# Kernel tuning notes

Measured on AMD Instinct MI355X. Metric: run time of the kernel, lower is better.

The kernel has to match this reference:

```python
import jax, jax.numpy as jnp
import numpy as np

B, N, D, P, H = 16, 1024, 512, 512, 8
E = P // H  # head dim = 64


def layer_norm(x, g, b, eps=1e-5):
    mu = jnp.mean(x, axis=-1, keepdims=True)
    var = jnp.var(x, axis=-1, keepdims=True)
    return (x - mu) * jax.lax.rsqrt(var + eps) * g + b


def setup_inputs() -> dict:
    key = jax.random.key(0)
    ks = jax.random.split(key, 12)
    s = 0.02
    inp = {
        "x": jax.random.normal(ks[0], (B, N, D), dtype=jnp.float32),
        "Wq": jax.random.normal(ks[1], (D, P), dtype=jnp.float32) * s,
        "bq": jnp.zeros((P,), jnp.float32),
        "Wk": jax.random.normal(ks[2], (D, P), dtype=jnp.float32) * s,
        "bk": jnp.zeros((P,), jnp.float32),
        "Wv": jax.random.normal(ks[3], (D, P), dtype=jnp.float32) * s,
        "bv": jnp.zeros((P,), jnp.float32),
        "Wo": jax.random.normal(ks[4], (P, D), dtype=jnp.float32) * s,
        "bo": jnp.zeros((D,), jnp.float32),
        "ln1_g": jnp.ones((D,), jnp.float32),
        "ln1_b": jnp.zeros((D,), jnp.float32),
        "W1": jax.random.normal(ks[5], (D, 4 * D), dtype=jnp.float32) * s,
        "b1": jnp.zeros((4 * D,), jnp.float32),
        "W2": jax.random.normal(ks[6], (4 * D, D), dtype=jnp.float32) * s,
        "b2": jnp.zeros((D,), jnp.float32),
        "ln2_g": jnp.ones((D,), jnp.float32),
        "ln2_b": jnp.zeros((D,), jnp.float32),
    }
    return inp


def reference(x, Wq, bq, Wk, bk, Wv, bv, Wo, bo, ln1_g, ln1_b, W1, b1, W2, b2, ln2_g, ln2_b):
    # dropout layers are identity in eval mode
    q = (x @ Wq + bq).reshape(B, N, H, E)
    k = (x @ Wk + bk).reshape(B, N, H, E)
    v = (x @ Wv + bv).reshape(B, N, H, E)
    scale = 1.0 / jnp.sqrt(jnp.float32(E))
    scores = jnp.einsum('blhe,bshe->bhls', q, k)  # [B,H,L,S]
    A = jax.nn.softmax(scale * scores, axis=-1)
    V = jnp.einsum('bhls,bshd->blhd', A, v).reshape(B, N, P)
    att = V @ Wo + bo
    x1 = layer_norm(x + att, ln1_g, ln1_b)
    # FFN: 1x1 convs over channel dim == per-token linears, exact GELU
    ff = jax.nn.gelu(x1 @ W1 + b1, approximate=False) @ W2 + b2
    return layer_norm(x1 + ff, ln2_g, ln2_b)
```

## Files before the change

kernel.cpp:

```cpp
#include <hip/hip_runtime.h>
#include <hip/hip_bf16.h>

typedef __hip_bfloat16 bf16;
typedef __bf16 bf16x8 __attribute__((ext_vector_type(8)));
typedef __bf16 bf16x4 __attribute__((ext_vector_type(4)));
typedef float f32x4 __attribute__((ext_vector_type(4)));

static __device__ __forceinline__ f32x4 mfma16(bf16x8 a, bf16x8 b, f32x4 c) {
  return __builtin_amdgcn_mfma_f32_16x16x32_bf16(a, b, c, 0, 0, 0);
}
static __device__ __forceinline__ bf16x8 ld8(const bf16* p) {
  return *reinterpret_cast<const bf16x8*>(p);
}

typedef __attribute__((address_space(1))) void gvoid;
typedef __attribute__((address_space(3))) void lvoid;
static __device__ __forceinline__ void gl2lds16(const bf16* g, bf16* l) {
  __builtin_amdgcn_global_load_lds((gvoid*)g, (lvoid*)l, 16, 0, 0);
}

__global__ __launch_bounds__(256) void cvt_prep(
    const float* __restrict__ x, bf16* __restrict__ xb,
    const float* __restrict__ Wq, const float* __restrict__ Wk,
    const float* __restrict__ Wv, const float* __restrict__ Wo,
    const float* __restrict__ W1, const float* __restrict__ W2,
    bf16* __restrict__ Wtqkv, bf16* __restrict__ WtO,
    bf16* __restrict__ Wt1, bf16* __restrict__ Wt2) {
  int blk = blockIdx.x;
  int tx = threadIdx.x, ty = threadIdx.y;
  if (blk < 8192) {
    int t = ty * 32 + tx;
    long i = (long)blk * 256 + t;
    float4 v = reinterpret_cast<const float4*>(x)[i];
    bf16x4 o;
    o[0] = __float2bfloat16(v.x); o[1] = __float2bfloat16(v.y);
    o[2] = __float2bfloat16(v.z); o[3] = __float2bfloat16(v.w);
    reinterpret_cast<bf16x4*>(xb)[i] = o;
    return;
  }
  int id = blk - 8192;
  const float* in;
  bf16* out;
  int K, N, n0, k0;
  if (id < 1024) {
    int which = id >> 8, t = id & 255;
    K = 512; N = 512;
    n0 = (t & 15) * 32; k0 = (t >> 4) * 32;
    if (which == 0)      { in = Wq; out = Wtqkv; }
    else if (which == 1) { in = Wk; out = Wtqkv + (size_t)512 * 512; }
    else if (which == 2) { in = Wv; out = Wtqkv + (size_t)1024 * 512; }
    else                 { in = Wo; out = WtO; }
  } else if (id < 2048) {
    int t = id - 1024;
    in = W1; out = Wt1; K = 512; N = 2048;
    n0 = (t & 63) * 32; k0 = (t >> 6) * 32;
  } else {
    int t = id - 2048;
    in = W2; out = Wt2; K = 2048; N = 512;
    n0 = (t & 15) * 32; k0 = (t >> 4) * 32;
  }
  __shared__ float tile[32][33];
#pragma unroll
  for (int j = 0; j < 32; j += 8)
    tile[ty + j][tx] = in[(long)(k0 + ty + j) * N + n0 + tx];
  __syncthreads();
#pragma unroll
  for (int j = 0; j < 32; j += 8)
    out[(long)(n0 + ty + j) * K + k0 + tx] = __float2bfloat16(tile[tx][ty + j]);
}

__global__ __launch_bounds__(256) void cvt_kernel(const float* __restrict__ in,
                                                  bf16* __restrict__ out) {
  long i = (long)blockIdx.x * 256 + threadIdx.x;
  float4 v = reinterpret_cast<const float4*>(in)[i];
  bf16x4 o;
  o[0] = __float2bfloat16(v.x); o[1] = __float2bfloat16(v.y);
  o[2] = __float2bfloat16(v.z); o[3] = __float2bfloat16(v.w);
  reinterpret_cast<bf16x4*>(out)[i] = o;
}

__global__ void prep_weights(const float* __restrict__ Wq, const float* __restrict__ Wk,
                             const float* __restrict__ Wv, const float* __restrict__ Wo,
                             const float* __restrict__ W1, const float* __restrict__ W2,
                             bf16* __restrict__ Wtqkv, bf16* __restrict__ WtO,
                             bf16* __restrict__ Wt1, bf16* __restrict__ Wt2) {
  int id = blockIdx.x;
  const float* in;
  bf16* out;
  int K, N, n0, k0;
  if (id < 1024) {
    int which = id >> 8, t = id & 255;
    K = 512; N = 512;
    n0 = (t & 15) * 32; k0 = (t >> 4) * 32;
    if (which == 0)      { in = Wq; out = Wtqkv; }
    else if (which == 1) { in = Wk; out = Wtqkv + (size_t)512 * 512; }
    else if (which == 2) { in = Wv; out = Wtqkv + (size_t)1024 * 512; }
    else                 { in = Wo; out = WtO; }
  } else if (id < 2048) {
    int t = id - 1024;
    in = W1; out = Wt1; K = 512; N = 2048;
    n0 = (t & 63) * 32; k0 = (t >> 6) * 32;
  } else {
    int t = id - 2048;
    in = W2; out = Wt2; K = 2048; N = 512;
    n0 = (t & 15) * 32; k0 = (t >> 4) * 32;
  }
  __shared__ float tile[32][33];
  int tx = threadIdx.x, ty = threadIdx.y;
#pragma unroll
  for (int j = 0; j < 32; j += 8)
    tile[ty + j][tx] = in[(long)(k0 + ty + j) * N + n0 + tx];
  __syncthreads();
#pragma unroll
  for (int j = 0; j < 32; j += 8)
    out[(long)(n0 + ty + j) * K + k0 + tx] = __float2bfloat16(tile[tx][ty + j]);
}

template <int MODE>
__global__ __launch_bounds__(256) void gemm_kernel(
    const bf16* __restrict__ A, const bf16* __restrict__ Wt,
    const float* __restrict__ b0, const float* __restrict__ b1_,
    const float* __restrict__ b2_, bf16* C0, bf16* C1, bf16* C2,
    int K, int ldc, int mmask, int mshift) {
  __shared__ alignas(16) bf16 As[3][128 * 32];
  __shared__ alignas(16) bf16 Bs[3][128 * 32];
  const int tid = threadIdx.x;
  const int wave = tid >> 6, lane = tid & 63;
  const int lr = lane & 15, lq = lane >> 4;
  const int L = blockIdx.x;
  const int m0 = (L & mmask) * 128, n0 = (L >> mshift) * 128;
  const int wm = (wave >> 1) * 64, wn = (wave & 1) * 64;

  const int srow0 = (wave * 2) * 16 + (lane >> 2);
  const int srow1 = (wave * 2 + 1) * 16 + (lane >> 2);
  const int scol = (lane & 3) * 8;
  const bf16* Ag0 = A + (long)(m0 + srow0) * K + scol;
  const bf16* Ag1 = A + (long)(m0 + srow1) * K + scol;
  const bf16* Bg0 = Wt + (long)(n0 + srow0) * K + scol;
  const bf16* Bg1 = Wt + (long)(n0 + srow1) * K + scol;
  const int so0 = (wave * 2) * 16 * 32;
  const int so1 = (wave * 2 + 1) * 16 * 32;

  f32x4 acc[4][4] = {};

  auto stage = [&](int k0, int buf) {
    gl2lds16(Ag0 + k0, &As[buf][so0]);
    gl2lds16(Ag1 + k0, &As[buf][so1]);
    gl2lds16(Bg0 + k0, &Bs[buf][so0]);
    gl2lds16(Bg1 + k0, &Bs[buf][so1]);
  };

  stage(0, 0);
  stage(32, 1);

  const int nk = K >> 5;
  int cur = 0, sb = 2;
  for (int t = 0; t < nk; ++t) {
    if (t < nk - 1) {
      asm volatile("s_waitcnt vmcnt(4)" ::: "memory");
    } else {
      asm volatile("s_waitcnt vmcnt(0)" ::: "memory");
    }
    __builtin_amdgcn_s_barrier();
    if (t < nk - 2) stage((t + 2) << 5, sb);

    bf16x8 af[4], bfr[4];
#pragma unroll
    for (int i = 0; i < 4; ++i) af[i] = ld8(&As[cur][(wm + i * 16 + lr) * 32 + lq * 8]);
#pragma unroll
    for (int j = 0; j < 4; ++j) bfr[j] = ld8(&Bs[cur][(wn + j * 16 + lr) * 32 + lq * 8]);
    if constexpr (MODE == 3) {
#pragma unroll
      for (int i = 0; i < 4; ++i)
#pragma unroll
        for (int j = 0; j < 4; ++j) acc[i][j] = mfma16(af[i], bfr[j], acc[i][j]);
    } else {
#pragma unroll
      for (int i = 0; i < 4; ++i)
#pragma unroll
        for (int j = 0; j < 4; ++j) acc[i][j] = mfma16(bfr[j], af[i], acc[i][j]);
    }

    cur = (cur == 2) ? 0 : cur + 1;
    sb = (sb == 2) ? 0 : sb + 1;
  }

  if constexpr (MODE == 3) {
#pragma unroll
    for (int i = 0; i < 4; ++i) {
      int row0 = m0 + wm + i * 16 + lq * 4;
      int bb = row0 >> 10, tok = row0 & 1023;
#pragma unroll
      for (int j = 0; j < 4; ++j) {
        int col = n0 + wn + j * 16 + lr;
        float bv = b0[col];
        int hh = col >> 6, e = col & 63;
        bf16x4 o;
#pragma unroll
        for (int rr = 0; rr < 4; ++rr) o[rr] = __float2bfloat16(acc[i][j][rr] + bv);
        *reinterpret_cast<bf16x4*>(
            &C0[(((long)((bb * 8 + hh) * 64 + e)) << 10) + tok]) = o;
      }
    }
  } else {
    const float* bias = b0;
    bf16* C = C0;
    int cb = n0;
    if (MODE == 2 && n0 >= 512) { bias = b1_; C = C1; cb = n0 - 512; }
#pragma unroll
    for (int i = 0; i < 4; ++i) {
      int row = m0 + wm + i * 16 + lr;
      long rb = (long)row * ldc;
#pragma unroll
      for (int j = 0; j < 4; ++j) {
        int col0 = cb + wn + j * 16 + lq * 4;
        f32x4 bv = *reinterpret_cast<const f32x4*>(&bias[col0]);
        bf16x4 o;
#pragma unroll
        for (int rr = 0; rr < 4; ++rr) {
          float v = acc[i][j][rr] + bv[rr];
          if (MODE == 1) v = 0.5f * v * (1.0f + erff(v * 0.70710678118654752f));
          o[rr] = __float2bfloat16(v);
        }
        *reinterpret_cast<bf16x4*>(&C[rb + col0]) = o;
      }
    }
  }
}

__global__ __launch_bounds__(256) void attn_fused(
    const bf16* __restrict__ Q, const bf16* __restrict__ Km,
    const bf16* __restrict__ Vt, bf16* __restrict__ O) {
  constexpr int SP = 72;
  __shared__ alignas(16) bf16 Pall[4][32 * SP];
  __shared__ alignas(16) bf16 Ks[2][2][64][32];
  __shared__ alignas(16) bf16 Vs[2][2][64][32];
  const int tid = threadIdx.x;
  const int wave = tid >> 6, lane = tid & 63;
  const int lr = lane & 15, lq = lane >> 4;
  const int L = blockIdx.x;
  const int bh = ((L >> 6) << 3) | (L & 7);
  const int qc = (L >> 3) & 7;
  const int h = bh & 7, b = bh >> 3;
  const int q0 = qc * 128 + wave * 32;
  bf16* P = Pall[wave];
  const float Cc = 0.18033688011112042f;

  bf16x8 qf[2][2];
#pragma unroll
  for (int qs = 0; qs < 2; ++qs) {
    const bf16* qrow = Q + (long)(b * 1024 + q0 + qs * 16 + lr) * 512 + h * 64;
    qf[qs][0] = ld8(qrow + lq * 8);
    qf[qs][1] = ld8(qrow + 32 + lq * 8);
  }
  const bf16* kbase = Km + (long)(b * 1024) * 512 + h * 64;
  const bf16* vbase = Vt + (long)((b * 8 + h) * 64) * 1024;

  const int sr = wave * 16 + (lane >> 2);
  const int sc = (lane & 3) * 8;
  const bf16* Kg = kbase + (long)sr * 512 + sc;
  const bf16* Vg = vbase + (long)sr * 1024 + sc;

  auto stage = [&](int kb, int p) {
#pragma unroll
    for (int kk = 0; kk < 2; ++kk)
      gl2lds16(Kg + (long)kb * 64 * 512 + kk * 32, &Ks[p][kk][wave * 16][0]);
#pragma unroll
    for (int kk = 0; kk < 2; ++kk)
      gl2lds16(Vg + kb * 64 + kk * 32, &Vs[p][kk][wave * 16][0]);
  };

  bf16x8 ones;
#pragma unroll
  for (int k = 0; k < 8; ++k) ones[k] = __float2bfloat16(1.0f);

  f32x4 oacc[2][4] = {};
  f32x4 lacc[2] = {};

  stage(0, 0);
  __syncthreads();

  int p = 0;
  for (int kb = 0; kb < 16; ++kb) {
    if (kb < 15) stage(kb + 1, p ^ 1);
#pragma unroll
    for (int kt = 0; kt < 4; ++kt) {
      bf16x8 kf0 = ld8(&Ks[p][0][kt * 16 + lr][lq * 8]);
      bf16x8 kf1 = ld8(&Ks[p][1][kt * 16 + lr][lq * 8]);
#pragma unroll
      for (int qs = 0; qs < 2; ++qs) {
        f32x4 t = {};
        t = mfma16(kf0, qf[qs][0], t);
        t = mfma16(kf1, qf[qs][1], t);
        bf16x4 pk;
#pragma unroll
        for (int rr = 0; rr < 4; ++rr) pk[rr] = __float2bfloat16(exp2f(t[rr] * Cc));
        *reinterpret_cast<bf16x4*>(&P[(qs * 16 + lr) * SP + kt * 16 + lq * 4]) = pk;
      }
    }
    __builtin_amdgcn_sched_barrier(0);
    bf16x8 pf[2][2];
#pragma unroll
    for (int qs = 0; qs < 2; ++qs) {
      pf[qs][0] = ld8(&P[(qs * 16 + lr) * SP + lq * 8]);
      pf[qs][1] = ld8(&P[(qs * 16 + lr) * SP + 32 + lq * 8]);
    }
#pragma unroll
    for (int qs = 0; qs < 2; ++qs) {
      lacc[qs] = mfma16(ones, pf[qs][0], lacc[qs]);
      lacc[qs] = mfma16(ones, pf[qs][1], lacc[qs]);
    }
#pragma unroll
    for (int j0 = 0; j0 < 4; ++j0) {
      bf16x8 vf0 = ld8(&Vs[p][0][j0 * 16 + lr][lq * 8]);
      bf16x8 vf1 = ld8(&Vs[p][1][j0 * 16 + lr][lq * 8]);
#pragma unroll
      for (int qs = 0; qs < 2; ++qs) {
        oacc[qs][j0] = mfma16(vf0, pf[qs][0], oacc[qs][j0]);
        oacc[qs][j0] = mfma16(vf1, pf[qs][1], oacc[qs][j0]);
      }
    }
    __builtin_amdgcn_sched_barrier(0);
    __syncthreads();
    p ^= 1;
  }

#pragma unroll
  for (int qs = 0; qs < 2; ++qs) {
    float lv = 1.0f / lacc[qs][0];
    bf16* orow = O + (long)(b * 1024 + q0 + qs * 16 + lr) * 512 + h * 64 + lq * 4;
#pragma unroll
    for (int j0 = 0; j0 < 4; ++j0) {
      bf16x4 o;
#pragma unroll
      for (int rr = 0; rr < 4; ++rr) o[rr] = __float2bfloat16(oacc[qs][j0][rr] * lv);
      *reinterpret_cast<bf16x4*>(&orow[j0 * 16]) = o;
    }
  }
}

__global__ __launch_bounds__(256) void attn_kernel(
    const bf16* Q, const bf16* __restrict__ Km,
    const bf16* __restrict__ Vt, bf16* O) {
  constexpr int SP = 72;
  __shared__ alignas(16) bf16 Pall[4][64 * SP];
  const int tid = threadIdx.x;
  const int wave = tid >> 6, lane = tid & 63;
  const int lr = lane & 15, lq = lane >> 4;
  const int L = blockIdx.x;
  const int bh = ((L >> 5) << 3) | (L & 7);
  const int qc = (L >> 3) & 3;
  const int h = bh & 7, b = bh >> 3;
  const int q0 = qc * 256 + wave * 64;
  bf16* P = Pall[wave];
  const float Cc = 0.18033688011112042f;

  bf16x8 qf[4][2];
#pragma unroll
  for (int qs = 0; qs < 4; ++qs) {
    const bf16* qrow = Q + (long)(b * 1024 + q0 + qs * 16 + lr) * 512 + h * 64;
    qf[qs][0] = ld8(qrow + lq * 8);
    qf[qs][1] = ld8(qrow + 32 + lq * 8);
  }
  const bf16* kbase = Km + (long)(b * 1024) * 512 + h * 64;
  const bf16* vbase = Vt + (long)((b * 8 + h) * 64) * 1024;

  bf16x8 ones;
#pragma unroll
  for (int k = 0; k < 8; ++k) ones[k] = __float2bfloat16(1.0f);

  f32x4 oacc[4][4] = {};
  f32x4 lacc[4] = {};

  for (int kb = 0; kb < 16; ++kb) {
#pragma unroll
    for (int kt = 0; kt < 4; ++kt) {
      const bf16* krow = kbase + (long)(kb * 64 + kt * 16 + lr) * 512;
      bf16x8 kf0 = ld8(krow + lq * 8);
      bf16x8 kf1 = ld8(krow + 32 + lq * 8);
#pragma unroll
      for (int qs = 0; qs < 4; ++qs) {
        f32x4 t = {};
        t = mfma16(kf0, qf[qs][0], t);
        t = mfma16(kf1, qf[qs][1], t);
        bf16x4 pk;
#pragma unroll
        for (int rr = 0; rr < 4; ++rr) pk[rr] = __float2bfloat16(exp2f(t[rr] * Cc));
        *reinterpret_cast<bf16x4*>(&P[(qs * 16 + lr) * SP + kt * 16 + lq * 4]) = pk;
      }
    }
    __builtin_amdgcn_sched_barrier(0);
    bf16x8 pf[4][2];
#pragma unroll
    for (int qs = 0; qs < 4; ++qs) {
      pf[qs][0] = ld8(&P[(qs * 16 + lr) * SP + lq * 8]);
      pf[qs][1] = ld8(&P[(qs * 16 + lr) * SP + 32 + lq * 8]);
    }
#pragma unroll
    for (int qs = 0; qs < 4; ++qs) {
      lacc[qs] = mfma16(pf[qs][0], ones, lacc[qs]);
      lacc[qs] = mfma16(pf[qs][1], ones, lacc[qs]);
    }
#pragma unroll
    for (int j0 = 0; j0 < 4; ++j0) {
      const bf16* vrow = vbase + (long)(j0 * 16 + lr) * 1024 + kb * 64;
      bf16x8 vf0 = ld8(vrow + lq * 8);
      bf16x8 vf1 = ld8(vrow + 32 + lq * 8);
#pragma unroll
      for (int qs = 0; qs < 4; ++qs) {
        oacc[qs][j0] = mfma16(pf[qs][0], vf0, oacc[qs][j0]);
        oacc[qs][j0] = mfma16(pf[qs][1], vf1, oacc[qs][j0]);
      }
    }
    __builtin_amdgcn_sched_barrier(0);
  }

#pragma unroll
  for (int qs = 0; qs < 4; ++qs)
#pragma unroll
    for (int rr = 0; rr < 4; ++rr) {
      float lv = 1.0f / lacc[qs][rr];
#pragma unroll
      for (int j0 = 0; j0 < 4; ++j0)
        O[(long)(b * 1024 + q0 + qs * 16 + lq * 4 + rr) * 512 + h * 64 + j0 * 16 + lr] =
            __float2bfloat16(oacc[qs][j0][rr] * lv);
    }
}

template <typename TO>
__global__ __launch_bounds__(256) void add_ln_kernel(
    const bf16* __restrict__ X, const bf16* __restrict__ Y,
    const float* __restrict__ g, const float* __restrict__ bb,
    TO* __restrict__ out) {
  const int lane = threadIdx.x & 63, wave = threadIdx.x >> 6;
  const long row = (long)blockIdx.x * 4 + wave;
  const long base = row * 512 + lane * 8;
  bf16x8 xv = ld8(X + base);
  bf16x8 yv = ld8(Y + base);
  float v[8];
  float s = 0.f, q = 0.f;
#pragma unroll
  for (int k = 0; k < 8; ++k) {
    v[k] = (float)xv[k] + (float)yv[k];
    s += v[k];
    q += v[k] * v[k];
  }
#pragma unroll
  for (int o = 32; o > 0; o >>= 1) {
    s += __shfl_down(s, o);
    q += __shfl_down(q, o);
  }
  s = __shfl(s, 0);
  q = __shfl(q, 0);
  float mean = s * (1.f / 512.f);
  float var = q * (1.f / 512.f) - mean * mean;
  float rs = rsqrtf(var + 1e-5f);
  f32x4 g0 = *reinterpret_cast<const f32x4*>(&g[lane * 8]);
  f32x4 g1 = *reinterpret_cast<const f32x4*>(&g[lane * 8 + 4]);
  f32x4 b0 = *reinterpret_cast<const f32x4*>(&bb[lane * 8]);
  f32x4 b1 = *reinterpret_cast<const f32x4*>(&bb[lane * 8 + 4]);
  float r[8];
#pragma unroll
  for (int k = 0; k < 4; ++k) {
    r[k]     = (v[k]     - mean) * rs * g0[k] + b0[k];
    r[k + 4] = (v[k + 4] - mean) * rs * g1[k] + b1[k];
  }
  if constexpr (sizeof(TO) == 2) {
    bf16x8 o;
#pragma unroll
    for (int k = 0; k < 8; ++k) o[k] = __float2bfloat16(r[k]);
    *reinterpret_cast<bf16x8*>(&out[base]) = o;
  } else {
    f32x4 o0, o1;
#pragma unroll
    for (int k = 0; k < 4; ++k) { o0[k] = r[k]; o1[k] = r[k + 4]; }
    *reinterpret_cast<f32x4*>(&out[base]) = o0;
    *reinterpret_cast<f32x4*>(&out[base + 4]) = o1;
  }
}

extern "C" void kernel_launch(void* const* d_in, const int* in_sizes, int n_in,
                              void* d_out, int out_size, void* d_ws, size_t ws_size,
                              hipStream_t stream) {
  const float* x    = (const float*)d_in[0];
  const float* Wq   = (const float*)d_in[1];
  const float* bq   = (const float*)d_in[2];
  const float* Wk   = (const float*)d_in[3];
  const float* bk   = (const float*)d_in[4];
  const float* Wv   = (const float*)d_in[5];
  const float* bv   = (const float*)d_in[6];
  const float* Wo   = (const float*)d_in[7];
  const float* bo   = (const float*)d_in[8];
  const float* ln1g = (const float*)d_in[9];
  const float* ln1b = (const float*)d_in[10];
  const float* W1   = (const float*)d_in[11];
  const float* b1   = (const float*)d_in[12];
  const float* W2   = (const float*)d_in[13];
  const float* b2   = (const float*)d_in[14];
  const float* ln2g = (const float*)d_in[15];
  const float* ln2b = (const float*)d_in[16];
  float* out = (float*)d_out;

  char* ws = (char*)d_ws;
  size_t off = 0;
  auto alloc = [&](size_t bytes) {
    char* p = ws + off;
    off += (bytes + 255) & ~(size_t)255;
    return (bf16*)p;
  };
  bf16* Wtqkv = alloc((size_t)1536 * 512 * 2);
  bf16* WtO   = alloc((size_t)512 * 512 * 2);
  bf16* Wt1   = alloc((size_t)512 * 2048 * 2);
  bf16* Wt2   = alloc((size_t)2048 * 512 * 2);
  const size_t SB = (size_t)16384 * 512 * 2;

  dim3 tb(32, 8);

  if (ws_size >= (size_t)104 * 1024 * 1024) {
    bf16* xb  = alloc(SB);
    bf16* kb  = alloc(SB);
    bf16* qb  = alloc(SB);
    bf16* vtb = alloc(SB);
    bf16* p0  = alloc(SB);
    bf16* p1  = alloc(SB);
    bf16* ff1 = qb;
    bf16* ff2 = xb;
    (void)p0; (void)p1;

    cvt_prep<<<11264, tb, 0, stream>>>(x, xb, Wq, Wk, Wv, Wo, W1, W2,
                                       Wtqkv, WtO, Wt1, Wt2);
    gemm_kernel<2><<<1024, 256, 0, stream>>>(xb, Wtqkv, bq, bk, nullptr,
                                             qb, kb, nullptr, 512, 512, 127, 7);
    gemm_kernel<3><<<512, 256, 0, stream>>>(xb, Wtqkv + (size_t)1024 * 512, bv,
                                            nullptr, nullptr, vtb, nullptr, nullptr,
                                            512, 512, 127, 7);
    attn_fused<<<1024, 256, 0, stream>>>(qb, kb, vtb, qb);
    gemm_kernel<0><<<512, 256, 0, stream>>>(qb, WtO, bo, nullptr, nullptr,
                                            vtb, nullptr, nullptr, 512, 512, 127, 7);
    add_ln_kernel<bf16><<<4096, 256, 0, stream>>>(xb, vtb, ln1g, ln1b, kb);
    gemm_kernel<1><<<2048, 256, 0, stream>>>(kb, Wt1, b1, nullptr, nullptr,
                                             ff1, nullptr, nullptr, 512, 2048, 127, 7);
    gemm_kernel<0><<<512, 256, 0, stream>>>(ff1, Wt2, b2, nullptr, nullptr,
                                            ff2, nullptr, nullptr, 2048, 512, 127, 7);
    add_ln_kernel<float><<<4096, 256, 0, stream>>>(kb, ff2, ln2g, ln2b, out);
  } else {
    bf16* xb  = alloc(SB);
    bf16* kb  = alloc(SB);
    bf16* qb  = alloc(SB);
    bf16* vtb = alloc(SB);
    bf16* fb  = alloc(SB / 2);
    bf16* ff1 = qb;

    cvt_kernel<<<8192, 256, 0, stream>>>(x, xb);
    prep_weights<<<3072, tb, 0, stream>>>(Wq, Wk, Wv, Wo, W1, W2,
                                          Wtqkv, WtO, Wt1, Wt2);
    gemm_kernel<2><<<1024, 256, 0, stream>>>(xb, Wtqkv, bq, bk, nullptr,
                                             qb, kb, nullptr, 512, 512, 127, 7);
    gemm_kernel<3><<<512, 256, 0, stream>>>(xb, Wtqkv + (size_t)1024 * 512, bv,
                                            nullptr, nullptr, vtb, nullptr, nullptr,
                                            512, 512, 127, 7);
    attn_kernel<<<512, 256, 0, stream>>>(qb, kb, vtb, qb);
    gemm_kernel<0><<<512, 256, 0, stream>>>(qb, WtO, bo, nullptr, nullptr,
                                            vtb, nullptr, nullptr, 512, 512, 127, 7);
    add_ln_kernel<bf16><<<4096, 256, 0, stream>>>(xb, vtb, ln1g, ln1b, kb);

    for (int hh = 0; hh < 2; ++hh) {
      const bf16* x1h = kb + (size_t)hh * 8192 * 512;
      gemm_kernel<1><<<1024, 256, 0, stream>>>(x1h, Wt1, b1, nullptr, nullptr,
                                               ff1, nullptr, nullptr, 512, 2048, 63, 6);
      gemm_kernel<0><<<256, 256, 0, stream>>>(ff1, Wt2, b2, nullptr, nullptr,
                                              fb, nullptr, nullptr, 2048, 512, 63, 6);
      add_ln_kernel<float><<<2048, 256, 0, stream>>>(x1h, fb, ln2g, ln2b,
                                                     out + (size_t)hh * 8192 * 512);
    }
  }
}
```

Before: 368.9 us.

## Add 256x256 GEMM tile kernel and fold softmax scale into Wq

Adds a 512-thread GEMM kernel with 256x256 output tiles and a three-stage LDS pipeline, used for the QK projection and the FFN up-projection with GELU. Larger tiles raise reuse per LDS load and cut the number of blocks. The softmax scale (log2e/sqrt(E)) is now folded into Wq and bq during weight prep, which removes a multiply per score in the attention kernels. Risks are lower occupancy and more register pressure from the 8x4 accumulator tile, and fewer blocks (256) for the QK GEMM than there are CUs.

```diff
diff --git a/kernel.cpp b/kernel.cpp
--- a/kernel.cpp
+++ b/kernel.cpp
@@ -18,12 +18,15 @@
 static __device__ __forceinline__ void gl2lds16(const bf16* g, bf16* l) {
   __builtin_amdgcn_global_load_lds((gvoid*)g, (lvoid*)l, 16, 0, 0);
 }
+
+#define CC_SCALE 0.18033688011112042f
 
 __global__ __launch_bounds__(256) void cvt_prep(
     const float* __restrict__ x, bf16* __restrict__ xb,
     const float* __restrict__ Wq, const float* __restrict__ Wk,
     const float* __restrict__ Wv, const float* __restrict__ Wo,
     const float* __restrict__ W1, const float* __restrict__ W2,
+    const float* __restrict__ bq, float* __restrict__ bqs,
     bf16* __restrict__ Wtqkv, bf16* __restrict__ WtO,
     bf16* __restrict__ Wt1, bf16* __restrict__ Wt2) {
   int blk = blockIdx.x;
@@ -38,15 +41,22 @@
     reinterpret_cast<bf16x4*>(xb)[i] = o;
     return;
   }
+  if (blk == 11264) {
+    int t = ty * 32 + tx;
+    bqs[t] = bq[t] * CC_SCALE;
+    bqs[t + 256] = bq[t + 256] * CC_SCALE;
+    return;
+  }
   int id = blk - 8192;
   const float* in;
   bf16* out;
   int K, N, n0, k0;
+  float scl = 1.0f;
   if (id < 1024) {
     int which = id >> 8, t = id & 255;
     K = 512; N = 512;
     n0 = (t & 15) * 32; k0 = (t >> 4) * 32;
-    if (which == 0)      { in = Wq; out = Wtqkv; }
+    if (which == 0)      { in = Wq; out = Wtqkv; scl = CC_SCALE; }
     else if (which == 1) { in = Wk; out = Wtqkv + (size_t)512 * 512; }
     else if (which == 2) { in = Wv; out = Wtqkv + (size_t)1024 * 512; }
     else                 { in = Wo; out = WtO; }
@@ -66,7 +76,7 @@
   __syncthreads();
 #pragma unroll
   for (int j = 0; j < 32; j += 8)
-    out[(long)(n0 + ty + j) * K + k0 + tx] = __float2bfloat16(tile[tx][ty + j]);
+    out[(long)(n0 + ty + j) * K + k0 + tx] = __float2bfloat16(tile[tx][ty + j] * scl);
 }
 
 __global__ __launch_bounds__(256) void cvt_kernel(const float* __restrict__ in,
@@ -82,17 +92,25 @@
 __global__ void prep_weights(const float* __restrict__ Wq, const float* __restrict__ Wk,
                              const float* __restrict__ Wv, const float* __restrict__ Wo,
                              const float* __restrict__ W1, const float* __restrict__ W2,
+                             const float* __restrict__ bq, float* __restrict__ bqs,
                              bf16* __restrict__ Wtqkv, bf16* __restrict__ WtO,
                              bf16* __restrict__ Wt1, bf16* __restrict__ Wt2) {
   int id = blockIdx.x;
+  int tx = threadIdx.x, ty = threadIdx.y;
+  if (id == 0) {
+    int t = ty * 32 + tx;
+    bqs[t] = bq[t] * CC_SCALE;
+    bqs[t + 256] = bq[t + 256] * CC_SCALE;
+  }
   const float* in;
   bf16* out;
   int K, N, n0, k0;
+  float scl = 1.0f;
   if (id < 1024) {
     int which = id >> 8, t = id & 255;
     K = 512; N = 512;
     n0 = (t & 15) * 32; k0 = (t >> 4) * 32;
-    if (which == 0)      { in = Wq; out = Wtqkv; }
+    if (which == 0)      { in = Wq; out = Wtqkv; scl = CC_SCALE; }
     else if (which == 1) { in = Wk; out = Wtqkv + (size_t)512 * 512; }
     else if (which == 2) { in = Wv; out = Wtqkv + (size_t)1024 * 512; }
     else                 { in = Wo; out = WtO; }
@@ -106,14 +124,13 @@
     n0 = (t & 15) * 32; k0 = (t >> 4) * 32;
   }
   __shared__ float tile[32][33];
-  int tx = threadIdx.x, ty = threadIdx.y;
 #pragma unroll
   for (int j = 0; j < 32; j += 8)
     tile[ty + j][tx] = in[(long)(k0 + ty + j) * N + n0 + tx];
   __syncthreads();
 #pragma unroll
   for (int j = 0; j < 32; j += 8)
-    out[(long)(n0 + ty + j) * K + k0 + tx] = __float2bfloat16(tile[tx][ty + j]);
+    out[(long)(n0 + ty + j) * K + k0 + tx] = __float2bfloat16(tile[tx][ty + j] * scl);
 }
 
 template <int MODE>
@@ -224,6 +241,90 @@
         }
         *reinterpret_cast<bf16x4*>(&C[rb + col0]) = o;
       }
+    }
+  }
+}
+
+template <int MODE>
+__global__ __launch_bounds__(512) void gemm256(
+    const bf16* __restrict__ A, const bf16* __restrict__ Wt,
+    const float* __restrict__ b0, const float* __restrict__ b1_,
+    bf16* C0, bf16* C1, int K, int ldc, int mmask, int mshift) {
+  __shared__ alignas(16) bf16 As[3][256 * 32];
+  __shared__ alignas(16) bf16 Bs[3][256 * 32];
+  const int tid = threadIdx.x;
+  const int wave = tid >> 6, lane = tid & 63;
+  const int lr = lane & 15, lq = lane >> 4;
+  const int L = blockIdx.x;
+  const int m0 = (L & mmask) * 256, n0 = (L >> mshift) * 256;
+  const int wm = (wave >> 2) * 128, wn = (wave & 3) * 64;
+
+  const int sr = tid >> 2;
+  const int sc = (tid & 3) * 8;
+  const bf16* Ag0 = A + (long)(m0 + sr) * K + sc;
+  const bf16* Ag1 = A + (long)(m0 + 128 + sr) * K + sc;
+  const bf16* Bg0 = Wt + (long)(n0 + sr) * K + sc;
+  const bf16* Bg1 = Wt + (long)(n0 + 128 + sr) * K + sc;
+  const int so0 = tid * 8;
+  const int so1 = (tid + 512) * 8;
+
+  f32x4 acc[8][4] = {};
+
+  auto stage = [&](int k0, int buf) {
+    gl2lds16(Ag0 + k0, &As[buf][so0]);
+    gl2lds16(Ag1 + k0, &As[buf][so1]);
+    gl2lds16(Bg0 + k0, &Bs[buf][so0]);
+    gl2lds16(Bg1 + k0, &Bs[buf][so1]);
+  };
+
+  stage(0, 0);
+  stage(32, 1);
+
+  const int nk = K >> 5;
+  int cur = 0, sb = 2;
+  for (int t = 0; t < nk; ++t) {
+    if (t < nk - 1) {
+      asm volatile("s_waitcnt vmcnt(4)" ::: "memory");
+    } else {
+      asm volatile("s_waitcnt vmcnt(0)" ::: "memory");
+    }
+    __builtin_amdgcn_s_barrier();
+    if (t < nk - 2) stage((t + 2) << 5, sb);
+
+    bf16x8 af[8], bfr[4];
+#pragma unroll
+    for (int i = 0; i < 8; ++i) af[i] = ld8(&As[cur][(wm + i * 16 + lr) * 32 + lq * 8]);
+#pragma unroll
+    for (int j = 0; j < 4; ++j) bfr[j] = ld8(&Bs[cur][(wn + j * 16 + lr) * 32 + lq * 8]);
+#pragma unroll
+    for (int i = 0; i < 8; ++i)
+#pragma unroll
+      for (int j = 0; j < 4; ++j) acc[i][j] = mfma16(bfr[j], af[i], acc[i][j]);
+
+    cur = (cur == 2) ? 0 : cur + 1;
+    sb = (sb == 2) ? 0 : sb + 1;
+  }
+
+  const float* bias = b0;
+  bf16* C = C0;
+  int cb = n0;
+  if (MODE == 2 && n0 >= 512) { bias = b1_; C = C1; cb = n0 - 512; }
+#pragma unroll
+  for (int i = 0; i < 8; ++i) {
+    int row = m0 + wm + i * 16 + lr;
+    long rb = (long)row * ldc;
+#pragma unroll
+    for (int j = 0; j < 4; ++j) {
+      int col0 = cb + wn + j * 16 + lq * 4;
+      f32x4 bv = *reinterpret_cast<const f32x4*>(&bias[col0]);
+      bf16x4 o;
+#pragma unroll
+      for (int rr = 0; rr < 4; ++rr) {
+        float v = acc[i][j][rr] + bv[rr];
+        if (MODE == 1) v = 0.5f * v * (1.0f + erff(v * 0.70710678118654752f));
+        o[rr] = __float2bfloat16(v);
+      }
+      *reinterpret_cast<bf16x4*>(&C[rb + col0]) = o;
     }
   }
 }
@@ -244,7 +345,6 @@
   const int h = bh & 7, b = bh >> 3;
   const int q0 = qc * 128 + wave * 32;
   bf16* P = Pall[wave];
-  const float Cc = 0.18033688011112042f;
 
   bf16x8 qf[2][2];
 #pragma unroll
@@ -294,7 +394,7 @@
         t = mfma16(kf1, qf[qs][1], t);
         bf16x4 pk;
 #pragma unroll
-        for (int rr = 0; rr < 4; ++rr) pk[rr] = __float2bfloat16(exp2f(t[rr] * Cc));
+        for (int rr = 0; rr < 4; ++rr) pk[rr] = __float2bfloat16(exp2f(t[rr]));
         *reinterpret_cast<bf16x4*>(&P[(qs * 16 + lr) * SP + kt * 16 + lq * 4]) = pk;
       }
     }
@@ -353,7 +453,6 @@
   const int h = bh & 7, b = bh >> 3;
   const int q0 = qc * 256 + wave * 64;
   bf16* P = Pall[wave];
-  const float Cc = 0.18033688011112042f;
 
   bf16x8 qf[4][2];
 #pragma unroll
@@ -385,7 +484,7 @@
         t = mfma16(kf1, qf[qs][1], t);
         bf16x4 pk;
 #pragma unroll
-        for (int rr = 0; rr < 4; ++rr) pk[rr] = __float2bfloat16(exp2f(t[rr] * Cc));
+        for (int rr = 0; rr < 4; ++rr) pk[rr] = __float2bfloat16(exp2f(t[rr]));
         *reinterpret_cast<bf16x4*>(&P[(qs * 16 + lr) * SP + kt * 16 + lq * 4]) = pk;
       }
     }
@@ -512,6 +611,7 @@
   bf16* WtO   = alloc((size_t)512 * 512 * 2);
   bf16* Wt1   = alloc((size_t)512 * 2048 * 2);
   bf16* Wt2   = alloc((size_t)2048 * 512 * 2);
+  float* bqs  = (float*)alloc((size_t)512 * 4);
   const size_t SB = (size_t)16384 * 512 * 2;
 
   dim3 tb(32, 8);
@@ -527,10 +627,10 @@
     bf16* ff2 = xb;
     (void)p0; (void)p1;
 
-    cvt_prep<<<11264, tb, 0, stream>>>(x, xb, Wq, Wk, Wv, Wo, W1, W2,
+    cvt_prep<<<11265, tb, 0, stream>>>(x, xb, Wq, Wk, Wv, Wo, W1, W2, bq, bqs,
                                        Wtqkv, WtO, Wt1, Wt2);
-    gemm_kernel<2><<<1024, 256, 0, stream>>>(xb, Wtqkv, bq, bk, nullptr,
-                                             qb, kb, nullptr, 512, 512, 127, 7);
+    gemm256<2><<<256, 512, 0, stream>>>(xb, Wtqkv, bqs, bk,
+                                        qb, kb, 512, 512, 63, 6);
     gemm_kernel<3><<<512, 256, 0, stream>>>(xb, Wtqkv + (size_t)1024 * 512, bv,
                                             nullptr, nullptr, vtb, nullptr, nullptr,
                                             512, 512, 127, 7);
@@ -538,8 +638,8 @@
     gemm_kernel<0><<<512, 256, 0, stream>>>(qb, WtO, bo, nullptr, nullptr,
                                             vtb, nullptr, nullptr, 512, 512, 127, 7);
     add_ln_kernel<bf16><<<4096, 256, 0, stream>>>(xb, vtb, ln1g, ln1b, kb);
-    gemm_kernel<1><<<2048, 256, 0, stream>>>(kb, Wt1, b1, nullptr, nullptr,
-                                             ff1, nullptr, nullptr, 512, 2048, 127, 7);
+    gemm256<1><<<512, 512, 0, stream>>>(kb, Wt1, b1, nullptr,
+                                        ff1, nullptr, 512, 2048, 63, 6);
     gemm_kernel<0><<<512, 256, 0, stream>>>(ff1, Wt2, b2, nullptr, nullptr,
                                             ff2, nullptr, nullptr, 2048, 512, 127, 7);
     add_ln_kernel<float><<<4096, 256, 0, stream>>>(kb, ff2, ln2g, ln2b, out);
@@ -552,9 +652,9 @@
     bf16* ff1 = qb;
 
     cvt_kernel<<<8192, 256, 0, stream>>>(x, xb);
-    prep_weights<<<3072, tb, 0, stream>>>(Wq, Wk, Wv, Wo, W1, W2,
+    prep_weights<<<3072, tb, 0, stream>>>(Wq, Wk, Wv, Wo, W1, W2, bq, bqs,
                                           Wtqkv, WtO, Wt1, Wt2);
-    gemm_kernel<2><<<1024, 256, 0, stream>>>(xb, Wtqkv, bq, bk, nullptr,
+    gemm_kernel<2><<<1024, 256, 0, stream>>>(xb, Wtqkv, bqs, bk, nullptr,
                                              qb, kb, nullptr, 512, 512, 127, 7);
     gemm_kernel<3><<<512, 256, 0, stream>>>(xb, Wtqkv + (size_t)1024 * 512, bv,
                                             nullptr, nullptr, vtb, nullptr, nullptr,
```

Measured after the change: 382.9 us. 3.8% more time.

## Swizzle LDS tiles to avoid bank conflicts and fold softmax scale into Wq

Applied to the files above, without the earlier changes.

Applies an XOR swizzle to the 16-byte column chunks that global_load_lds writes into LDS in the GEMM and attention kernels. The reads apply the matching XOR, which targets LDS bank conflicts on the bf16x8 fragment loads. Separately, the exp2 softmax constant is pre-multiplied into Wq and bq during weight prep, which removes one multiply per score in the attention inner loop. The swizzle must match between writer and reader lanes to stay correct, and scaling Wq before the bf16 cast slightly changes rounding.

```diff
diff --git a/kernel.cpp b/kernel.cpp
--- a/kernel.cpp
+++ b/kernel.cpp
@@ -18,12 +18,16 @@
 static __device__ __forceinline__ void gl2lds16(const bf16* g, bf16* l) {
   __builtin_amdgcn_global_load_lds((gvoid*)g, (lvoid*)l, 16, 0, 0);
 }
+
+#define CC_SCALE 0.18033688011112042f
+
 
 __global__ __launch_bounds__(256) void cvt_prep(
     const float* __restrict__ x, bf16* __restrict__ xb,
     const float* __restrict__ Wq, const float* __restrict__ Wk,
     const float* __restrict__ Wv, const float* __restrict__ Wo,
     const float* __restrict__ W1, const float* __restrict__ W2,
+    const float* __restrict__ bq, float* __restrict__ bqs,
     bf16* __restrict__ Wtqkv, bf16* __restrict__ WtO,
     bf16* __restrict__ Wt1, bf16* __restrict__ Wt2) {
   int blk = blockIdx.x;
@@ -38,15 +42,22 @@
     reinterpret_cast<bf16x4*>(xb)[i] = o;
     return;
   }
+  if (blk == 11264) {
+    int t = ty * 32 + tx;
+    bqs[t] = bq[t] * CC_SCALE;
+    bqs[t + 256] = bq[t + 256] * CC_SCALE;
+    return;
+  }
   int id = blk - 8192;
   const float* in;
   bf16* out;
   int K, N, n0, k0;
+  float scl = 1.0f;
   if (id < 1024) {
     int which = id >> 8, t = id & 255;
     K = 512; N = 512;
     n0 = (t & 15) * 32; k0 = (t >> 4) * 32;
-    if (which == 0)      { in = Wq; out = Wtqkv; }
+    if (which == 0)      { in = Wq; out = Wtqkv; scl = CC_SCALE; }
     else if (which == 1) { in = Wk; out = Wtqkv + (size_t)512 * 512; }
     else if (which == 2) { in = Wv; out = Wtqkv + (size_t)1024 * 512; }
     else                 { in = Wo; out = WtO; }
@@ -66,7 +77,7 @@
   __syncthreads();
 #pragma unroll
   for (int j = 0; j < 32; j += 8)
-    out[(long)(n0 + ty + j) * K + k0 + tx] = __float2bfloat16(tile[tx][ty + j]);
+    out[(long)(n0 + ty + j) * K + k0 + tx] = __float2bfloat16(tile[tx][ty + j] * scl);
 }
 
 __global__ __launch_bounds__(256) void cvt_kernel(const float* __restrict__ in,
@@ -82,17 +93,25 @@
 __global__ void prep_weights(const float* __restrict__ Wq, const float* __restrict__ Wk,
                              const float* __restrict__ Wv, const float* __restrict__ Wo,
                              const float* __restrict__ W1, const float* __restrict__ W2,
+                             const float* __restrict__ bq, float* __restrict__ bqs,
                              bf16* __restrict__ Wtqkv, bf16* __restrict__ WtO,
                              bf16* __restrict__ Wt1, bf16* __restrict__ Wt2) {
   int id = blockIdx.x;
+  int tx = threadIdx.x, ty = threadIdx.y;
+  if (id == 0) {
+    int t = ty * 32 + tx;
+    bqs[t] = bq[t] * CC_SCALE;
+    bqs[t + 256] = bq[t + 256] * CC_SCALE;
+  }
   const float* in;
   bf16* out;
   int K, N, n0, k0;
+  float scl = 1.0f;
   if (id < 1024) {
     int which = id >> 8, t = id & 255;
     K = 512; N = 512;
     n0 = (t & 15) * 32; k0 = (t >> 4) * 32;
-    if (which == 0)      { in = Wq; out = Wtqkv; }
+    if (which == 0)      { in = Wq; out = Wtqkv; scl = CC_SCALE; }
     else if (which == 1) { in = Wk; out = Wtqkv + (size_t)512 * 512; }
     else if (which == 2) { in = Wv; out = Wtqkv + (size_t)1024 * 512; }
     else                 { in = Wo; out = WtO; }
@@ -106,14 +125,13 @@
     n0 = (t & 15) * 32; k0 = (t >> 4) * 32;
   }
   __shared__ float tile[32][33];
-  int tx = threadIdx.x, ty = threadIdx.y;
 #pragma unroll
   for (int j = 0; j < 32; j += 8)
     tile[ty + j][tx] = in[(long)(k0 + ty + j) * N + n0 + tx];
   __syncthreads();
 #pragma unroll
   for (int j = 0; j < 32; j += 8)
-    out[(long)(n0 + ty + j) * K + k0 + tx] = __float2bfloat16(tile[tx][ty + j]);
+    out[(long)(n0 + ty + j) * K + k0 + tx] = __float2bfloat16(tile[tx][ty + j] * scl);
 }
 
 template <int MODE>
@@ -133,13 +151,14 @@
 
   const int srow0 = (wave * 2) * 16 + (lane >> 2);
   const int srow1 = (wave * 2 + 1) * 16 + (lane >> 2);
-  const int scol = (lane & 3) * 8;
+  const int scol = (((lane & 3) ^ ((lane >> 3) & 3))) * 8;
   const bf16* Ag0 = A + (long)(m0 + srow0) * K + scol;
   const bf16* Ag1 = A + (long)(m0 + srow1) * K + scol;
   const bf16* Bg0 = Wt + (long)(n0 + srow0) * K + scol;
   const bf16* Bg1 = Wt + (long)(n0 + srow1) * K + scol;
   const int so0 = (wave * 2) * 16 * 32;
   const int so1 = (wave * 2 + 1) * 16 * 32;
+  const int xr = (lr >> 1) & 3;
 
   f32x4 acc[4][4] = {};
 
@@ -166,9 +185,11 @@
 
     bf16x8 af[4], bfr[4];
 #pragma unroll
-    for (int i = 0; i < 4; ++i) af[i] = ld8(&As[cur][(wm + i * 16 + lr) * 32 + lq * 8]);
-#pragma unroll
-    for (int j = 0; j < 4; ++j) bfr[j] = ld8(&Bs[cur][(wn + j * 16 + lr) * 32 + lq * 8]);
+    for (int i = 0; i < 4; ++i)
+      af[i] = ld8(&As[cur][(wm + i * 16 + lr) * 32 + (lq ^ xr) * 8]);
+#pragma unroll
+    for (int j = 0; j < 4; ++j)
+      bfr[j] = ld8(&Bs[cur][(wn + j * 16 + lr) * 32 + (lq ^ xr) * 8]);
     if constexpr (MODE == 3) {
 #pragma unroll
       for (int i = 0; i < 4; ++i)
@@ -244,7 +265,6 @@
   const int h = bh & 7, b = bh >> 3;
   const int q0 = qc * 128 + wave * 32;
   bf16* P = Pall[wave];
-  const float Cc = 0.18033688011112042f;
 
   bf16x8 qf[2][2];
 #pragma unroll
@@ -257,9 +277,10 @@
   const bf16* vbase = Vt + (long)((b * 8 + h) * 64) * 1024;
 
   const int sr = wave * 16 + (lane >> 2);
-  const int sc = (lane & 3) * 8;
+  const int sc = (((lane & 3) ^ ((lane >> 3) & 3))) * 8;
   const bf16* Kg = kbase + (long)sr * 512 + sc;
   const bf16* Vg = vbase + (long)sr * 1024 + sc;
+  const int xr = (lr >> 1) & 3;
 
   auto stage = [&](int kb, int p) {
 #pragma unroll
@@ -285,8 +306,8 @@
     if (kb < 15) stage(kb + 1, p ^ 1);
 #pragma unroll
     for (int kt = 0; kt < 4; ++kt) {
-      bf16x8 kf0 = ld8(&Ks[p][0][kt * 16 + lr][lq * 8]);
-      bf16x8 kf1 = ld8(&Ks[p][1][kt * 16 + lr][lq * 8]);
+      bf16x8 kf0 = ld8(&Ks[p][0][kt * 16 + lr][(lq ^ xr) * 8]);
+      bf16x8 kf1 = ld8(&Ks[p][1][kt * 16 + lr][(lq ^ xr) * 8]);
 #pragma unroll
       for (int qs = 0; qs < 2; ++qs) {
         f32x4 t = {};
@@ -294,7 +315,7 @@
         t = mfma16(kf1, qf[qs][1], t);
         bf16x4 pk;
 #pragma unroll
-        for (int rr = 0; rr < 4; ++rr) pk[rr] = __float2bfloat16(exp2f(t[rr] * Cc));
+        for (int rr = 0; rr < 4; ++rr) pk[rr] = __float2bfloat16(exp2f(t[rr]));
         *reinterpret_cast<bf16x4*>(&P[(qs * 16 + lr) * SP + kt * 16 + lq * 4]) = pk;
       }
     }
@@ -312,8 +333,8 @@
     }
 #pragma unroll
     for (int j0 = 0; j0 < 4; ++j0) {
-      bf16x8 vf0 = ld8(&Vs[p][0][j0 * 16 + lr][lq * 8]);
-      bf16x8 vf1 = ld8(&Vs[p][1][j0 * 16 + lr][lq * 8]);
+      bf16x8 vf0 = ld8(&Vs[p][0][j0 * 16 + lr][(lq ^ xr) * 8]);
+      bf16x8 vf1 = ld8(&Vs[p][1][j0 * 16 + lr][(lq ^ xr) * 8]);
 #pragma unroll
       for (int qs = 0; qs < 2; ++qs) {
         oacc[qs][j0] = mfma16(vf0, pf[qs][0], oacc[qs][j0]);
@@ -353,7 +374,6 @@
   const int h = bh & 7, b = bh >> 3;
   const int q0 = qc * 256 + wave * 64;
   bf16* P = Pall[wave];
-  const float Cc = 0.18033688011112042f;
 
   bf16x8 qf[4][2];
 #pragma unroll
@@ -385,7 +405,7 @@
         t = mfma16(kf1, qf[qs][1], t);
         bf16x4 pk;
 #pragma unroll
-        for (int rr = 0; rr < 4; ++rr) pk[rr] = __float2bfloat16(exp2f(t[rr] * Cc));
+        for (int rr = 0; rr < 4; ++rr) pk[rr] = __float2bfloat16(exp2f(t[rr]));
         *reinterpret_cast<bf16x4*>(&P[(qs * 16 + lr) * SP + kt * 16 + lq * 4]) = pk;
       }
     }
@@ -512,6 +532,7 @@
   bf16* WtO   = alloc((size_t)512 * 512 * 2);
   bf16* Wt1   = alloc((size_t)512 * 2048 * 2);
   bf16* Wt2   = alloc((size_t)2048 * 512 * 2);
+  float* bqs  = (float*)alloc((size_t)512 * 4);
   const size_t SB = (size_t)16384 * 512 * 2;
 
   dim3 tb(32, 8);
@@ -527,9 +548,9 @@
     bf16* ff2 = xb;
     (void)p0; (void)p1;
 
-    cvt_prep<<<11264, tb, 0, stream>>>(x, xb, Wq, Wk, Wv, Wo, W1, W2,
+    cvt_prep<<<11265, tb, 0, stream>>>(x, xb, Wq, Wk, Wv, Wo, W1, W2, bq, bqs,
                                        Wtqkv, WtO, Wt1, Wt2);
-    gemm_kernel<2><<<1024, 256, 0, stream>>>(xb, Wtqkv, bq, bk, nullptr,
+    gemm_kernel<2><<<1024, 256, 0, stream>>>(xb, Wtqkv, bqs, bk, nullptr,
                                              qb, kb, nullptr, 512, 512, 127, 7);
     gemm_kernel<3><<<512, 256, 0, stream>>>(xb, Wtqkv + (size_t)1024 * 512, bv,
                                             nullptr, nullptr, vtb, nullptr, nullptr,
@@ -552,9 +573,9 @@
     bf16* ff1 = qb;
 
     cvt_kernel<<<8192, 256, 0, stream>>>(x, xb);
-    prep_weights<<<3072, tb, 0, stream>>>(Wq, Wk, Wv, Wo, W1, W2,
+    prep_weights<<<3072, tb, 0, stream>>>(Wq, Wk, Wv, Wo, W1, W2, bq, bqs,
                                           Wtqkv, WtO, Wt1, Wt2);
-    gemm_kernel<2><<<1024, 256, 0, stream>>>(xb, Wtqkv, bq, bk, nullptr,
+    gemm_kernel<2><<<1024, 256, 0, stream>>>(xb, Wtqkv, bqs, bk, nullptr,
                                              qb, kb, nullptr, 512, 512, 127, 7);
     gemm_kernel<3><<<512, 256, 0, stream>>>(xb, Wtqkv + (size_t)1024 * 512, bv,
                                             nullptr, nullptr, vtb, nullptr, nullptr,
```

Result: no change. 365.2 us (-1.0%).
